# Performance work log

Measured on AMD Instinct MI355X. Metric: run time of the kernel, lower is better.

Reference implementation:

```python
import jax, jax.numpy as jnp
import numpy as np

N = 50000          # total nodes in batch
E = 800000         # total edges (avg degree 16)
G = 512            # number of graphs in batch
H = 64             # hidden_channels
L = 5              # num_layers
C_IN = 1           # in_channels
NUM_CLASSES = 2
BN_EPS = 1e-5


def setup_inputs() -> dict:
    key = jax.random.key(0)
    ks = jax.random.split(key, 12)
    x = jax.random.normal(ks[0], (N, C_IN), dtype=jnp.float32)
    edge_index = jax.random.randint(ks[1], (2, E), 0, N, dtype=jnp.int64)
    batch = jnp.sort(jax.random.randint(ks[2], (N,), 0, G, dtype=jnp.int64))
    s = 0.1
    # GINConv MLP params: layer0 input is C_IN, layers 1..4 input is H
    w1_0 = jax.random.normal(ks[3], (C_IN, H), dtype=jnp.float32) * s
    w1_rest = jax.random.normal(ks[4], (L - 1, H, H), dtype=jnp.float32) * s
    b1 = jax.random.normal(ks[5], (L, H), dtype=jnp.float32) * s
    gamma_mlp = jnp.ones((L, H), dtype=jnp.float32)
    beta_mlp = jnp.zeros((L, H), dtype=jnp.float32)
    w2 = jax.random.normal(ks[6], (L, H, H), dtype=jnp.float32) * s
    b2 = jax.random.normal(ks[7], (L, H), dtype=jnp.float32) * s
    # outer per-layer BatchNorm (BasicGNN norm) params
    gamma = jnp.ones((L, H), dtype=jnp.float32)
    beta = jnp.zeros((L, H), dtype=jnp.float32)
    lin_w = jax.random.normal(ks[8], (C_IN + H * L, NUM_CLASSES), dtype=jnp.float32) * s
    lin_b = jnp.zeros((NUM_CLASSES,), dtype=jnp.float32)
    return dict(x=x, edge_index=edge_index, batch=batch, w1_0=w1_0,
                w1_rest=w1_rest, b1=b1, gamma_mlp=gamma_mlp, beta_mlp=beta_mlp,
                w2=w2, b2=b2, gamma=gamma, beta=beta, lin_w=lin_w, lin_b=lin_b)


def _bn(h, g, b):
    # training-mode batch norm over the node axis (biased variance, as torch)
    mu = h.mean(axis=0)
    var = h.var(axis=0)
    return (h - mu) * jax.lax.rsqrt(var + BN_EPS) * g + b


def _gin_backbone(x, src, dst, w1_0, w1_rest, b1, gm, bm, w2, b2, go, bo):
    h = x
    outs = []
    for l in range(L):  # fixed small layer count
        agg = jax.ops.segment_sum(h[src], dst, num_segments=N)  # sum_{j->i} h_j
        z = h + agg  # (1+eps)*h_i + agg, eps=0
        w1 = w1_0 if l == 0 else w1_rest[l - 1]
        z = z @ w1 + b1[l]
        z = jax.nn.relu(_bn(z, gm[l], bm[l]))   # MLP inner norm+act
        z = z @ w2[l] + b2[l]
        z = jax.nn.relu(_bn(z, go[l], bo[l]))   # BasicGNN norm+act (jk set)
        h = z
        outs.append(h)
    return jnp.concatenate(outs, axis=1)  # jk='cat' -> [N, H*L]


def reference(x, edge_index, batch, w1_0, w1_rest, b1, gamma_mlp, beta_mlp,
              w2, b2, gamma, beta, lin_w, lin_b):
    src, dst = edge_index[0], edge_index[1]
    node_desc = _gin_backbone(x, src, dst, w1_0, w1_rest, b1,
                              gamma_mlp, beta_mlp, w2, b2, gamma, beta)
    graph_desc = jax.ops.segment_sum(node_desc, batch, num_segments=G)  # [G, H*L]
    first_desc = jax.ops.segment_sum(x, batch, num_segments=G)          # [G, C_IN]
    gdesc = jnp.concatenate((first_desc, graph_desc), axis=1)           # [G, C_IN+H*L]
    # final dropout is identity in eval mode
    return gdesc @ lin_w + lin_b
```

## Files before the change

kernel.cpp:

```cpp
#include <hip/hip_runtime.h>

#define NN 50000
#define NE 800000
#define NG 512
#define HC 64
#define NL 5
#define GD_COLS 321
#define BN_EPS 1e-5f
#define DEG_CAP 64

typedef unsigned short bf16_t;
typedef unsigned int uiv4 __attribute__((ext_vector_type(4)));
typedef __attribute__((ext_vector_type(8))) short short8v;
typedef __attribute__((ext_vector_type(4))) float f32x4;
typedef __attribute__((ext_vector_type(4))) unsigned uint4v;

static __device__ __forceinline__ unsigned f2bfbits(float f) {
    unsigned u = __float_as_uint(f);
    return (u + 0x7FFFu + ((u >> 16) & 1u)) >> 16;
}
static __device__ __forceinline__ bf16_t f2bf(float f) { return (bf16_t)f2bfbits(f); }
static __device__ __forceinline__ float bf2f(bf16_t h) {
    return __uint_as_float(((unsigned)h) << 16);
}
static __device__ __forceinline__ float bflo(unsigned w) { return __uint_as_float(w << 16); }
static __device__ __forceinline__ float bfhi(unsigned w) {
    return __uint_as_float(w & 0xffff0000u);
}

static __device__ __forceinline__ void mfma_gemm_phase(
    const unsigned* zw, const unsigned* wsm, const float* __restrict__ bias,
    bf16_t* __restrict__ out, float* __restrict__ statsOut, float (*redS)[64],
    float (*redQ)[64], int r0, int t, int lane, int wid) {
    int l15 = lane & 15, l4 = lane >> 4;
    int tr = wid >> 1;
    int tc0 = (wid & 1) * 2;
    f32x4 d0 = {0.f, 0.f, 0.f, 0.f}, d1 = {0.f, 0.f, 0.f, 0.f};
    const unsigned* arow = &zw[(tr * 16 + l15) * 33];
    const unsigned* brow0 = &wsm[(tc0 * 16 + l15) * 33];
    const unsigned* brow1 = &wsm[((tc0 + 1) * 16 + l15) * 33];
#pragma unroll
    for (int kc = 0; kc < 2; ++kc) {
        int kb = kc * 16 + l4 * 4;
        uint4v aw = {arow[kb], arow[kb + 1], arow[kb + 2], arow[kb + 3]};
        uint4v bw0 = {brow0[kb], brow0[kb + 1], brow0[kb + 2], brow0[kb + 3]};
        uint4v bw1 = {brow1[kb], brow1[kb + 1], brow1[kb + 2], brow1[kb + 3]};
        short8v af = __builtin_bit_cast(short8v, aw);
        d0 = __builtin_amdgcn_mfma_f32_16x16x32_bf16(af, __builtin_bit_cast(short8v, bw0), d0,
                                                     0, 0, 0);
        d1 = __builtin_amdgcn_mfma_f32_16x16x32_bf16(af, __builtin_bit_cast(short8v, bw1), d1,
                                                     0, 0, 0);
    }
    int c0 = tc0 * 16 + l15, c1 = c0 + 16;
    float bv0 = bias[c0], bv1 = bias[c1];
    float s0 = 0.f, q0 = 0.f, s1 = 0.f, q1 = 0.f;
#pragma unroll
    for (int j = 0; j < 4; ++j) {
        int gr = r0 + tr * 16 + l4 * 4 + j;
        if (gr < NN) {
            float v0 = d0[j] + bv0, v1 = d1[j] + bv1;
            out[(size_t)gr * HC + c0] = f2bf(v0);
            out[(size_t)gr * HC + c1] = f2bf(v1);
            s0 += v0;
            q0 += v0 * v0;
            s1 += v1;
            q1 += v1 * v1;
        }
    }
    s0 += __shfl_xor(s0, 16); s0 += __shfl_xor(s0, 32);
    q0 += __shfl_xor(q0, 16); q0 += __shfl_xor(q0, 32);
    s1 += __shfl_xor(s1, 16); s1 += __shfl_xor(s1, 32);
    q1 += __shfl_xor(q1, 16); q1 += __shfl_xor(q1, 32);
    if (l4 == 0) { redS[wid][c0] = s0; redQ[wid][c0] = q0; }
    else if (l4 == 1) { redS[wid][c1] = s1; redQ[wid][c1] = q1; }
    else if (l4 == 2) { redS[wid][c0 ^ 32] = 0.f; redQ[wid][c0 ^ 32] = 0.f; }
    else { redS[wid][c1 ^ 32] = 0.f; redQ[wid][c1 ^ 32] = 0.f; }
    __syncthreads();
    if (t < 64) {
        float ts = 0.f, t2 = 0.f;
#pragma unroll
        for (int k = 0; k < 8; ++k) {
            ts += redS[k][t];
            t2 += redQ[k][t];
        }
        atomicAdd(&statsOut[t], ts);
        atomicAdd(&statsOut[64 + t], t2);
    }
}

__global__ void scatter_kernel(const int* __restrict__ ei, int* __restrict__ cnt,
                               unsigned short* __restrict__ ssrc, float* __restrict__ stats,
                               float* __restrict__ gdesc) {
    int gt = blockIdx.x * blockDim.x + threadIdx.x;
    int total = gridDim.x * blockDim.x;
    for (int i = gt; i < NL * 256; i += total) stats[i] = 0.f;
    for (int i = gt; i < NG * GD_COLS; i += total) gdesc[i] = 0.f;
    if (gt < NE) {
        int s = ei[gt];
        int d = ei[NE + gt];
        int pos = atomicAdd(&cnt[d], 1);
        if (pos < DEG_CAP) ssrc[(d << 6) + pos] = (unsigned short)s;
    }
}

__global__ __launch_bounds__(256) void layer0_kernel(
    const float* __restrict__ x, const int* __restrict__ cnt,
    const unsigned short* __restrict__ ssrc, const float* __restrict__ w,
    const float* __restrict__ bias, const int* __restrict__ batch, float* __restrict__ gdesc,
    bf16_t* __restrict__ y, float* __restrict__ stats) {
    __shared__ float z0p[256];
    __shared__ float z0s[64];
    int t = threadIdx.x, lane = t & 63, wid = t >> 6;
    int r0 = blockIdx.x * 64;
    if (t < 64) {
        int i = r0 + t;
        if (i < NN) atomicAdd(&gdesc[batch[i] * GD_COLS], x[i]);
    }
    {
        int node = t >> 2, sub = t & 3;
        int i = r0 + node;
        float acc = 0.f;
        if (i < NN) {
            int deg = cnt[i];
            if (deg > DEG_CAP) deg = DEG_CAP;
            int pa = i << 6;
            for (int p = sub; p < deg; p += 4) acc += x[ssrc[pa + p]];
            if (sub == 0) acc += x[i];
        }
        z0p[t] = acc;
    }
    __syncthreads();
    if (t < 64) z0s[t] = z0p[4 * t] + z0p[4 * t + 1] + z0p[4 * t + 2] + z0p[4 * t + 3];
    __syncthreads();
    float wv = w[lane], bv = bias[lane];
    float s = 0.f, s2 = 0.f;
    for (int j = 0; j < 16; ++j) {
        int r = r0 + wid * 16 + j;
        if (r < NN) {
            float v = z0s[wid * 16 + j] * wv + bv;
            y[r * HC + lane] = f2bf(v);
            s += v;
            s2 += v * v;
        }
    }
    __shared__ float ls[256], ls2[256];
    ls[t] = s;
    ls2[t] = s2;
    __syncthreads();
    if (wid == 0) {
        float ts = ls[lane] + ls[64 + lane] + ls[128 + lane] + ls[192 + lane];
        float t2 = ls2[lane] + ls2[64 + lane] + ls2[128 + lane] + ls2[192 + lane];
        atomicAdd(&stats[lane], ts);
        atomicAdd(&stats[64 + lane], t2);
    }
}

__global__ __launch_bounds__(512, 2) void gather_gemm_kernel(
    const bf16_t* __restrict__ u, const float* __restrict__ statsPrev,
    const float* __restrict__ gPrev, const float* __restrict__ bPrev,
    const int* __restrict__ cnt, const unsigned short* __restrict__ ssrc,
    const float* __restrict__ w, const float* __restrict__ bias, const int* __restrict__ batch,
    float* __restrict__ gdesc, int layerPrev, bf16_t* __restrict__ out,
    float* __restrict__ statsOut) {
    __shared__ unsigned zw[64 * 33];
    __shared__ unsigned wsm[64 * 33];
    __shared__ float a1[64], s1[64];
    __shared__ float redS[8][64], redQ[8][64];
    int t = threadIdx.x, lane = t & 63, wid = t >> 6;
    int r0 = blockIdx.x * 64;
    int li = lane & 7;
    int gq = lane >> 3;
    int gbase = lane & 56;
    int nB = r0 + wid * 8 + gq;
    uiv4 myidx;
    myidx[0] = 0; myidx[1] = 0; myidx[2] = 0; myidx[3] = 0;
    uiv4 selfv;
    selfv[0] = 0; selfv[1] = 0; selfv[2] = 0; selfv[3] = 0;
    int degB = 0;
    if (nB < NN) {
        degB = cnt[nB];
        if (degB > DEG_CAP) degB = DEG_CAP;
        myidx = *(const uiv4*)&ssrc[((size_t)nB << 6) + li * 8];
        selfv = *(const uiv4*)&u[(size_t)nB * HC + li * 8];
    }
    if (t < 64) {
        float mu = statsPrev[t] * (1.0f / NN);
        float var = statsPrev[64 + t] * (1.0f / NN) - mu * mu;
        float a = gPrev[t] * rsqrtf(var + BN_EPS);
        a1[t] = a;
        s1[t] = bPrev[t] - mu * a;
    }
    for (int idx = t; idx < 2048; idx += 512) {
        int kk = idx >> 6, c = idx & 63;
        unsigned lo = f2bfbits(w[(2 * kk) * 64 + c]);
        unsigned hi = f2bfbits(w[(2 * kk + 1) * 64 + c]);
        wsm[c * 33 + kk] = lo | (hi << 16);
    }
    __syncthreads();
    {
        float a8[8], s8[8];
#pragma unroll
        for (int c = 0; c < 8; ++c) {
            a8[c] = a1[li * 8 + c];
            s8[c] = s1[li * 8 + c];
        }
        float acc[8];
        if (nB < NN) {
            acc[0] = fmaxf(bflo(selfv[0]) * a8[0] + s8[0], 0.f);
            acc[1] = fmaxf(bfhi(selfv[0]) * a8[1] + s8[1], 0.f);
            acc[2] = fmaxf(bflo(selfv[1]) * a8[2] + s8[2], 0.f);
            acc[3] = fmaxf(bfhi(selfv[1]) * a8[3] + s8[3], 0.f);
            acc[4] = fmaxf(bflo(selfv[2]) * a8[4] + s8[4], 0.f);
            acc[5] = fmaxf(bfhi(selfv[2]) * a8[5] + s8[5], 0.f);
            acc[6] = fmaxf(bflo(selfv[3]) * a8[6] + s8[6], 0.f);
            acc[7] = fmaxf(bfhi(selfv[3]) * a8[7] + s8[7], 0.f);
        } else {
#pragma unroll
            for (int c = 0; c < 8; ++c) acc[c] = 0.f;
        }
        if (degB > 0) {
            uiv4 rv[8];
            int cntA = degB < 8 ? degB : 8;
            {
                unsigned w0 = __shfl(myidx[0], gbase);
                unsigned w1 = __shfl(myidx[1], gbase);
                unsigned w2 = __shfl(myidx[2], gbase);
                unsigned w3 = __shfl(myidx[3], gbase);
                int id[8] = {(int)(w0 & 0xffff), (int)(w0 >> 16), (int)(w1 & 0xffff),
                             (int)(w1 >> 16),    (int)(w2 & 0xffff), (int)(w2 >> 16),
                             (int)(w3 & 0xffff), (int)(w3 >> 16)};
#pragma unroll
                for (int e = 0; e < 8; ++e)
                    rv[e] = *(const uiv4*)&u[(size_t)id[e] * HC + li * 8];
            }
            for (int b = 1; cntA > 0; ++b) {
                uiv4 nv[8];
                int cntB = 0;
                if (b * 8 < degB) {
                    unsigned w0 = __shfl(myidx[0], gbase + b);
                    unsigned w1 = __shfl(myidx[1], gbase + b);
                    unsigned w2 = __shfl(myidx[2], gbase + b);
                    unsigned w3 = __shfl(myidx[3], gbase + b);
                    int id[8] = {(int)(w0 & 0xffff), (int)(w0 >> 16), (int)(w1 & 0xffff),
                                 (int)(w1 >> 16),    (int)(w2 & 0xffff), (int)(w2 >> 16),
                                 (int)(w3 & 0xffff), (int)(w3 >> 16)};
#pragma unroll
                    for (int e = 0; e < 8; ++e)
                        nv[e] = *(const uiv4*)&u[(size_t)id[e] * HC + li * 8];
                    cntB = degB - b * 8;
                    if (cntB > 8) cntB = 8;
                }
#pragma unroll
                for (int e = 0; e < 8; ++e) {
                    float v0 = fmaxf(bflo(rv[e][0]) * a8[0] + s8[0], 0.f);
                    float v1 = fmaxf(bfhi(rv[e][0]) * a8[1] + s8[1], 0.f);
                    float v2 = fmaxf(bflo(rv[e][1]) * a8[2] + s8[2], 0.f);
                    float v3 = fmaxf(bfhi(rv[e][1]) * a8[3] + s8[3], 0.f);
                    float v4 = fmaxf(bflo(rv[e][2]) * a8[4] + s8[4], 0.f);
                    float v5 = fmaxf(bfhi(rv[e][2]) * a8[5] + s8[5], 0.f);
                    float v6 = fmaxf(bflo(rv[e][3]) * a8[6] + s8[6], 0.f);
                    float v7 = fmaxf(bfhi(rv[e][3]) * a8[7] + s8[7], 0.f);
                    if (e < cntA) {
                        acc[0] += v0;
                        acc[1] += v1;
                        acc[2] += v2;
                        acc[3] += v3;
                        acc[4] += v4;
                        acc[5] += v5;
                        acc[6] += v6;
                        acc[7] += v7;
                    }
                }
#pragma unroll
                for (int e = 0; e < 8; ++e) rv[e] = nv[e];
                cntA = cntB;
            }
        }
        int lr = wid * 8 + gq;
        unsigned* zp = &zw[lr * 33 + li * 4];
        zp[0] = f2bfbits(acc[0]) | (f2bfbits(acc[1]) << 16);
        zp[1] = f2bfbits(acc[2]) | (f2bfbits(acc[3]) << 16);
        zp[2] = f2bfbits(acc[4]) | (f2bfbits(acc[5]) << 16);
        zp[3] = f2bfbits(acc[6]) | (f2bfbits(acc[7]) << 16);
    }
    {
        float av = a1[lane], sv = s1[lane];
        int col = 1 + layerPrev * HC + lane;
        float gacc = 0.f;
        int cur = -1;
        for (int j = 0; j < 8; ++j) {
            int gr = r0 + wid * 8 + j;
            if (gr < NN) {
                float hv = fmaxf(bf2f(u[(size_t)gr * HC + lane]) * av + sv, 0.f);
                int gid = batch[gr];
                if (gid != cur) {
                    if (cur >= 0) atomicAdd(&gdesc[cur * GD_COLS + col], gacc);
                    cur = gid;
                    gacc = 0.f;
                }
                gacc += hv;
            }
        }
        if (cur >= 0) atomicAdd(&gdesc[cur * GD_COLS + col], gacc);
    }
    __syncthreads();
    mfma_gemm_phase(zw, wsm, bias, out, statsOut, redS, redQ, r0, t, lane, wid);
}

__global__ __launch_bounds__(512) void gemm64_norm_kernel(
    const bf16_t* __restrict__ in, const float* __restrict__ w, const float* __restrict__ bias,
    const float* __restrict__ statsIn, const float* __restrict__ gIn,
    const float* __restrict__ bIn, bf16_t* __restrict__ out, float* __restrict__ statsOut) {
    __shared__ unsigned zw[64 * 33];
    __shared__ unsigned wsm[64 * 33];
    __shared__ float a1[64], s1[64];
    __shared__ float redS[8][64], redQ[8][64];
    int t = threadIdx.x, lane = t & 63, wid = t >> 6;
    int r0 = blockIdx.x * 64;
    if (t < 64) {
        float mu = statsIn[t] * (1.0f / NN);
        float var = statsIn[64 + t] * (1.0f / NN) - mu * mu;
        float a = gIn[t] * rsqrtf(var + BN_EPS);
        a1[t] = a;
        s1[t] = bIn[t] - mu * a;
    }
    for (int idx = t; idx < 2048; idx += 512) {
        int kk = idx >> 6, c = idx & 63;
        unsigned lo = f2bfbits(w[(2 * kk) * 64 + c]);
        unsigned hi = f2bfbits(w[(2 * kk + 1) * 64 + c]);
        wsm[c * 33 + kk] = lo | (hi << 16);
    }
    __syncthreads();
    for (int idx = t; idx < 2048; idx += 512) {
        int r = idx >> 5, kk = idx & 31;
        int gr = r0 + r;
        unsigned zword = 0u;
        if (gr < NN) {
            unsigned word = *(const unsigned*)&in[(size_t)gr * HC + 2 * kk];
            float v0 = fmaxf(bflo(word) * a1[2 * kk] + s1[2 * kk], 0.f);
            float v1 = fmaxf(bfhi(word) * a1[2 * kk + 1] + s1[2 * kk + 1], 0.f);
            zword = f2bfbits(v0) | (f2bfbits(v1) << 16);
        }
        zw[r * 33 + kk] = zword;
    }
    __syncthreads();
    mfma_gemm_phase(zw, wsm, bias, out, statsOut, redS, redQ, r0, t, lane, wid);
}

#define CHK 16
__global__ void gdesc_last_kernel(const bf16_t* __restrict__ u, const float* __restrict__ stats,
                                  const float* __restrict__ g, const float* __restrict__ b,
                                  const int* __restrict__ batch, float* __restrict__ gdesc,
                                  int layer) {
    int lane = threadIdx.x & 63;
    int wid = threadIdx.x >> 6;
    int i0 = (blockIdx.x * 4 + wid) * CHK;
    if (i0 >= NN) return;
    float mu = stats[lane] * (1.0f / NN);
    float var = stats[64 + lane] * (1.0f / NN) - mu * mu;
    float a = g[lane] * rsqrtf(var + BN_EPS);
    float s = b[lane] - mu * a;
    int col = 1 + layer * HC + lane;
    float acc = 0.f;
    int cur = -1;
    int iend = i0 + CHK;
    if (iend > NN) iend = NN;
    for (int i = i0; i < iend; ++i) {
        int gid = batch[i];
        if (gid != cur) {
            if (cur >= 0) atomicAdd(&gdesc[cur * GD_COLS + col], acc);
            cur = gid;
            acc = 0.f;
        }
        acc += fmaxf(bf2f(u[i * HC + lane]) * a + s, 0.f);
    }
    if (cur >= 0) atomicAdd(&gdesc[cur * GD_COLS + col], acc);
}

__global__ void final_gemm_kernel(const float* __restrict__ gdesc, const float* __restrict__ lw,
                                  const float* __restrict__ lb, float* __restrict__ out) {
    int g = blockIdx.x;
    int lane = threadIdx.x;
    float a0 = 0.f, a1 = 0.f;
    for (int j = lane; j < GD_COLS; j += 64) {
        float v = gdesc[g * GD_COLS + j];
        a0 += v * lw[j * 2 + 0];
        a1 += v * lw[j * 2 + 1];
    }
    for (int off = 32; off > 0; off >>= 1) {
        a0 += __shfl_down(a0, off);
        a1 += __shfl_down(a1, off);
    }
    if (lane == 0) {
        out[g * 2 + 0] = a0 + lb[0];
        out[g * 2 + 1] = a1 + lb[1];
    }
}

extern "C" void kernel_launch(void* const* d_in, const int* in_sizes, int n_in, void* d_out,
                              int out_size, void* d_ws, size_t ws_size, hipStream_t stream) {
    const float* x = (const float*)d_in[0];
    const int* ei = (const int*)d_in[1];
    const int* batch = (const int*)d_in[2];
    const float* w1_0 = (const float*)d_in[3];
    const float* w1_rest = (const float*)d_in[4];
    const float* b1 = (const float*)d_in[5];
    const float* gm = (const float*)d_in[6];
    const float* bm = (const float*)d_in[7];
    const float* w2 = (const float*)d_in[8];
    const float* b2 = (const float*)d_in[9];
    const float* go = (const float*)d_in[10];
    const float* bo = (const float*)d_in[11];
    const float* lw = (const float*)d_in[12];
    const float* lb = (const float*)d_in[13];
    float* out = (float*)d_out;

    float* stats = (float*)d_ws;
    float* gdesc = stats + NL * 256;
    bf16_t* ybuf = (bf16_t*)(gdesc + (size_t)NG * GD_COLS + 64);
    bf16_t* ubuf = ybuf + (size_t)NN * HC;
    int* cnt = (int*)(ubuf + (size_t)NN * HC);
    unsigned short* ssrc = (unsigned short*)(cnt + NN);

    hipMemsetAsync(cnt, 0, NN * sizeof(int), stream);

    scatter_kernel<<<(NE + 255) / 256, 256, 0, stream>>>(ei, cnt, ssrc, stats, gdesc);

    layer0_kernel<<<(NN + 63) / 64, 256, 0, stream>>>(x, cnt, ssrc, w1_0, b1, batch, gdesc, ybuf,
                                                      stats);
    gemm64_norm_kernel<<<(NN + 63) / 64, 512, 0, stream>>>(ybuf, w2, b2, stats, gm, bm, ubuf,
                                                           stats + 128);
    for (int l = 1; l < NL; ++l) {
        float* st1 = stats + l * 256;
        float* st2 = st1 + 128;
        float* stPrev = stats + (l - 1) * 256 + 128;
        gather_gemm_kernel<<<(NN + 63) / 64, 512, 0, stream>>>(
            ubuf, stPrev, go + (l - 1) * HC, bo + (l - 1) * HC, cnt, ssrc,
            w1_rest + (size_t)(l - 1) * HC * HC, b1 + l * HC, batch, gdesc, l - 1, ybuf, st1);
        gemm64_norm_kernel<<<(NN + 63) / 64, 512, 0, stream>>>(
            ybuf, w2 + (size_t)l * HC * HC, b2 + l * HC, st1, gm + l * HC, bm + l * HC, ubuf, st2);
    }
    gdesc_last_kernel<<<(NN + 4 * CHK - 1) / (4 * CHK), 256, 0, stream>>>(
        ubuf, stats + 4 * 256 + 128, go + 4 * HC, bo + 4 * HC, batch, gdesc, 4);
    final_gemm_kernel<<<NG, 64, 0, stream>>>(gdesc, lw, lb, out);
}
```

Baseline: 451.9 us.

## Build CSR adjacency via two-pass bucketed binning instead of global atomics

Replaces the per-edge global-atomic scatter into the padded adjacency table with two passes. First, edges are binned by destination bucket of 256 nodes, using shared-memory staging and a few global atomics per bucket. Second, one block per bucket builds its 256-node adjacency table in LDS and writes it out with coalesced vector stores. This cuts global atomic contention and scattered 2-byte writes, at the cost of an extra kernel launch and intermediate traffic through a buffer aliased onto ybuf. Overflow caps (CAPB, 64 per node) could drop edges on skewed degree distributions.

```diff
diff --git a/kernel.cpp b/kernel.cpp
--- a/kernel.cpp
+++ b/kernel.cpp
@@ -8,6 +8,10 @@
 #define GD_COLS 321
 #define BN_EPS 1e-5f
 #define DEG_CAP 64
+
+#define NBK 196
+#define CAPB 5120
+#define LCAP 64
 
 typedef unsigned short bf16_t;
 typedef unsigned int uiv4 __attribute__((ext_vector_type(4)));
@@ -88,18 +92,78 @@
     }
 }
 
-__global__ void scatter_kernel(const int* __restrict__ ei, int* __restrict__ cnt,
-                               unsigned short* __restrict__ ssrc, float* __restrict__ stats,
-                               float* __restrict__ gdesc) {
-    int gt = blockIdx.x * blockDim.x + threadIdx.x;
-    int total = gridDim.x * blockDim.x;
+__global__ __launch_bounds__(256) void bin_kernel(const int* __restrict__ ei,
+                                                  unsigned* __restrict__ ebuf,
+                                                  int* __restrict__ bcnt,
+                                                  float* __restrict__ stats,
+                                                  float* __restrict__ gdesc) {
+    __shared__ unsigned lbin[NBK][LCAP];
+    __shared__ int lcnt[NBK];
+    int t = threadIdx.x;
+    int gt = blockIdx.x * 256 + t;
+    int total = gridDim.x * 256;
     for (int i = gt; i < NL * 256; i += total) stats[i] = 0.f;
     for (int i = gt; i < NG * GD_COLS; i += total) gdesc[i] = 0.f;
-    if (gt < NE) {
-        int s = ei[gt];
-        int d = ei[NE + gt];
-        int pos = atomicAdd(&cnt[d], 1);
-        if (pos < DEG_CAP) ssrc[(d << 6) + pos] = (unsigned short)s;
+    for (int b = t; b < NBK; b += 256) lcnt[b] = 0;
+    __syncthreads();
+    int base = blockIdx.x * 4096;
+#pragma unroll
+    for (int i = 0; i < 16; ++i) {
+        int e = base + i * 256 + t;
+        if (e < NE) {
+            int s = ei[e];
+            int d = ei[NE + e];
+            int bkt = d >> 8;
+            unsigned enc = (unsigned)s | ((unsigned)(d & 255) << 16);
+            int pos = atomicAdd(&lcnt[bkt], 1);
+            if (pos < LCAP) lbin[bkt][pos] = enc;
+            else {
+                int gpos = atomicAdd(&bcnt[bkt], 1);
+                if (gpos < CAPB) ebuf[(size_t)bkt * CAPB + gpos] = enc;
+            }
+        }
+    }
+    __syncthreads();
+    int lane = t & 63, wid = t >> 6;
+    for (int bkt = wid; bkt < NBK; bkt += 4) {
+        int n = lcnt[bkt];
+        if (n > LCAP) n = LCAP;
+        int gbase = 0;
+        if (lane == 0 && n > 0) gbase = atomicAdd(&bcnt[bkt], n);
+        gbase = __shfl(gbase, 0);
+        for (int wq = lane; wq < n; wq += 64) {
+            int gp = gbase + wq;
+            if (gp < CAPB) ebuf[(size_t)bkt * CAPB + gp] = lbin[bkt][wq];
+        }
+    }
+}
+
+__global__ __launch_bounds__(256) void fill_kernel(const unsigned* __restrict__ ebuf,
+                                                   const int* __restrict__ bcnt,
+                                                   int* __restrict__ cnt,
+                                                   unsigned short* __restrict__ ssrc) {
+    __shared__ int c256[256];
+    __shared__ uiv4 tblv[2048];
+    unsigned short* tbl = (unsigned short*)tblv;
+    int t = threadIdx.x;
+    int b = blockIdx.x;
+    c256[t] = 0;
+    __syncthreads();
+    int blen = bcnt[b];
+    if (blen > CAPB) blen = CAPB;
+    for (int i = t; i < blen; i += 256) {
+        unsigned e = ebuf[(size_t)b * CAPB + i];
+        int dlo = e >> 16;
+        int pos = atomicAdd(&c256[dlo], 1);
+        if (pos < 64) tbl[dlo * 64 + pos] = (unsigned short)(e & 0xffffu);
+    }
+    __syncthreads();
+    int nb = b << 8;
+    if (nb + t < NN) cnt[nb + t] = c256[t];
+    uiv4* dst = (uiv4*)&ssrc[(size_t)nb << 6];
+    for (int i = t; i < 2048; i += 256) {
+        int node = nb + (i >> 3);
+        if (node < NN) dst[i] = tblv[i];
     }
 }
 
@@ -421,10 +485,13 @@
     bf16_t* ubuf = ybuf + (size_t)NN * HC;
     int* cnt = (int*)(ubuf + (size_t)NN * HC);
     unsigned short* ssrc = (unsigned short*)(cnt + NN);
-
-    hipMemsetAsync(cnt, 0, NN * sizeof(int), stream);
-
-    scatter_kernel<<<(NE + 255) / 256, 256, 0, stream>>>(ei, cnt, ssrc, stats, gdesc);
+    int* bcnt = (int*)(ssrc + (size_t)NN * 64);
+    unsigned* ebuf = (unsigned*)ybuf;
+
+    hipMemsetAsync(bcnt, 0, NBK * sizeof(int), stream);
+
+    bin_kernel<<<(NE + 4095) / 4096, 256, 0, stream>>>(ei, ebuf, bcnt, stats, gdesc);
+    fill_kernel<<<NBK, 256, 0, stream>>>(ebuf, bcnt, cnt, ssrc);
 
     layer0_kernel<<<(NN + 63) / 64, 256, 0, stream>>>(x, cnt, ssrc, w1_0, b1, batch, gdesc, ybuf,
                                                       stats);
```

After: 604.0 us. +33.7%, slower.
